# Optimization experiments

Measured on AMD Instinct MI355X. Metric: run time of the kernel, lower is better.

## Reference

```python
import jax, jax.numpy as jnp
import numpy as np

N = 12000       # num nodes
E = 384000      # num edges (avg degree 32)
F_IN = 512      # num_feats
H = 64          # gnn_hid_dim (== anchor_dim)
C = 7           # num_cls
SIGMA = 1.0


def setup_inputs() -> dict:
    key = jax.random.key(0)
    ks = jax.random.split(key, 9)
    scale = lambda fan_in: 1.0 / np.sqrt(fan_in)
    return {
        "x": jax.random.normal(ks[0], (N, F_IN), dtype=jnp.float32),
        "W1": jax.random.normal(ks[1], (F_IN, H), dtype=jnp.float32) * scale(F_IN),
        "b1": jnp.zeros((H,), dtype=jnp.float32),
        "W2": jax.random.normal(ks[2], (H, H), dtype=jnp.float32) * scale(H),
        "b2": jnp.zeros((H,), dtype=jnp.float32),
        "aux": jax.random.normal(ks[3], (H,), dtype=jnp.float32),
        "clf_W": jax.random.normal(ks[4], (2 * H, C), dtype=jnp.float32) * scale(2 * H),
        "clf_b": jnp.zeros((C,), dtype=jnp.float32),
        "edge_index": jax.random.randint(ks[5], (2, E), 0, N, dtype=jnp.int64),
    }


def gcn_conv(x, W, b, src, dst, n):
    # GCNConv: D^{-1/2} (A + I) D^{-1/2} X W + b, with self-loops
    h = x @ W                                                   # [N, out]
    deg = jax.ops.segment_sum(jnp.ones(src.shape[0], h.dtype), dst,
                              num_segments=n) + 1.0             # +1 for self-loop
    inv_sqrt = jax.lax.rsqrt(deg)
    norm = inv_sqrt[src] * inv_sqrt[dst]                        # [E]
    agg = jax.ops.segment_sum(h[src] * norm[:, None], dst, num_segments=n)
    agg = agg + h / deg[:, None]                                # self-loop term (norm = 1/deg)
    return agg + b


def reference(x, W1, b1, W2, b2, aux, clf_W, clf_b, edge_index):
    src, dst = edge_index[0], edge_index[1]
    n = x.shape[0]
    h = jax.nn.relu(gcn_conv(x, W1, b1, src, dst, n))
    h = gcn_conv(h, W2, b2, src, dst, n)                        # [N, H]
    # kernel aggregate: pairwise Gaussian kernel on cosine scores
    a = aux / jnp.maximum(jnp.linalg.norm(aux), 1e-12)          # F.normalize
    hn = jnp.maximum(jnp.linalg.norm(h, axis=-1), 1e-8)         # cosine_similarity eps
    score = (h @ a) / hn                                        # [N]
    diff = score[None, :] - score[:, None]                      # [N, N]
    kappa = jnp.exp(-(diff * diff) / (SIGMA * SIGMA))           # [N, N]
    z = (kappa @ h) / jnp.sum(kappa, axis=1, keepdims=True)     # [N, H]
    return jnp.concatenate([h, z], axis=-1) @ clf_W + clf_b     # [N, C]
```

## Files before the change

### kernel.cpp

```cpp
#include <hip/hip_runtime.h>
#include <hip/hip_bf16.h>

#define N_NODES 12000
#define N_EDGES 384000
#define F_IN 512
#define H 64
#define C_CLS 7
#define KTERMS 16
#define PAD 96
#define CSTR 32
#define MOM_BLKS 192
#define NB 4

__device__ __forceinline__ float wred_f(float x) {
    #pragma unroll
    for (int o = 32; o > 0; o >>= 1) x += __shfl_xor(x, o);
    return x;
}

__global__ __launch_bounds__(256) void init_k(int* __restrict__ cur,
                                              double* __restrict__ M,
                                              double* __restrict__ m0) {
    int i = blockIdx.x * 256 + threadIdx.x;
    if (i < N_NODES) cur[i * CSTR] = 0;
    if (i < KTERMS * 64) M[i] = 0.0;
    if (i < KTERMS) m0[i] = 0.0;
}

__global__ __launch_bounds__(256) void k1_gemm_fill(const float* __restrict__ x,
                                                    const float* __restrict__ W1,
                                                    const int* __restrict__ ei,
                                                    float* __restrict__ hbuf,
                                                    int* __restrict__ cur,
                                                    int* __restrict__ csrc) {
    const int b = blockIdx.x, t = threadIdx.x;
    if (b < 750) {
        __shared__ float xsT[64 * 19];
        __shared__ float wsm[64 * 64];
        const int tx = t & 15, ty = t >> 4;
        const int i0 = b * 16;
        float acc[4] = {};
        for (int k0 = 0; k0 < F_IN; k0 += 64) {
            {
                float4 v = *(const float4*)(x + (size_t)(i0 + ty) * F_IN + k0 + tx * 4);
                xsT[(tx * 4 + 0) * 19 + ty] = v.x;
                xsT[(tx * 4 + 1) * 19 + ty] = v.y;
                xsT[(tx * 4 + 2) * 19 + ty] = v.z;
                xsT[(tx * 4 + 3) * 19 + ty] = v.w;
            }
            #pragma unroll
            for (int q = 0; q < 4; ++q) {
                int idx = t + q * 256;
                int r = idx >> 4, c4 = idx & 15;
                *(float4*)(&wsm[r * 64 + c4 * 4]) =
                    *(const float4*)(W1 + (size_t)(k0 + r) * H + c4 * 4);
            }
            __syncthreads();
            #pragma unroll
            for (int kk = 0; kk < 64; ++kk) {
                float a = xsT[kk * 19 + ty];
                float4 bb = *(const float4*)(&wsm[kk * 64 + tx * 4]);
                acc[0] += a * bb.x; acc[1] += a * bb.y;
                acc[2] += a * bb.z; acc[3] += a * bb.w;
            }
            __syncthreads();
        }
        *(float4*)(hbuf + (size_t)(i0 + ty) * H + tx * 4) =
            make_float4(acc[0], acc[1], acc[2], acc[3]);
    } else {
        for (int e = (b - 750) * 256 + t; e < N_EDGES; e += 250 * 256) {
            int s = ei[e];
            int d = ei[N_EDGES + e];
            int pos = atomicAdd(&cur[d * CSTR], 1);
            if (pos < PAD) csrc[d * PAD + pos] = s;
        }
    }
}

__global__ __launch_bounds__(256) void agg1_k(const float* __restrict__ hbuf,
                                              const float* __restrict__ b1,
                                              const int* __restrict__ cur,
                                              const int* __restrict__ csrc,
                                              float* __restrict__ h1) {
    __shared__ int2 sPair[NB * PAD];
    __shared__ int sDeg[NB];
    __shared__ float sIsd[NB];
    const int t = threadIdx.x, f = t & 63, w = t >> 6;
    const int base = blockIdx.x * NB;
    if (t < NB) {
        int d = cur[(base + t) * CSTR];
        sDeg[t] = min(d, PAD);
        sIsd[t] = rsqrtf((float)d + 1.f);
    }
    __syncthreads();
    for (int idx = t; idx < NB * PAD; idx += 256) {
        int n = idx / PAD, e = idx - n * PAD;
        if (e < sDeg[n]) {
            int s = csrc[(base + n) * PAD + e];
            float ws_ = rsqrtf((float)cur[s * CSTR] + 1.f);
            sPair[idx] = make_int2(s, __float_as_int(ws_));
        }
    }
    __syncthreads();
    const int i = base + w;
    const int deg = sDeg[w];
    const float isd = sIsd[w];
    const int2* pp = sPair + w * PAD;
    float acc = 0.f;
    int e = 0;
    for (; e + 4 <= deg; e += 4) {
        int2 p0 = pp[e], p1 = pp[e + 1], p2 = pp[e + 2], p3 = pp[e + 3];
        acc += hbuf[p0.x * H + f] * __int_as_float(p0.y)
             + hbuf[p1.x * H + f] * __int_as_float(p1.y)
             + hbuf[p2.x * H + f] * __int_as_float(p2.y)
             + hbuf[p3.x * H + f] * __int_as_float(p3.y);
    }
    for (; e < deg; ++e) {
        int2 p = pp[e];
        acc += hbuf[p.x * H + f] * __int_as_float(p.y);
    }
    float res = (acc + hbuf[i * H + f] * isd) * isd + b1[f];
    h1[i * H + f] = fmaxf(res, 0.f);
}

__global__ __launch_bounds__(256) void agg2_k(const float* __restrict__ h1,
                                              const float* __restrict__ W2,
                                              const float* __restrict__ b2,
                                              const float* __restrict__ aux,
                                              const int* __restrict__ cur,
                                              const int* __restrict__ csrc,
                                              float* __restrict__ h2,
                                              float* __restrict__ score) {
    __shared__ float w2s[64 * 64];
    __shared__ int2 sPair[NB * PAD];
    __shared__ int sDeg[NB];
    __shared__ float sIsd[NB];
    __shared__ float anorm[64];
    __shared__ float gsh[NB * 64];
    const int t = threadIdx.x, f = t & 63, w = t >> 6;
    const int base = blockIdx.x * NB;
    #pragma unroll
    for (int q = 0; q < 4; ++q) {
        int idx = t + q * 256;
        int r = idx >> 4, c4 = idx & 15;
        *(float4*)(&w2s[r * 64 + c4 * 4]) = *(const float4*)(W2 + r * H + c4 * 4);
    }
    if (t < NB) {
        int d = cur[(base + t) * CSTR];
        sDeg[t] = min(d, PAD);
        sIsd[t] = rsqrtf((float)d + 1.f);
    }
    if (t < 64) {
        float av = aux[t];
        anorm[t] = av * rsqrtf(fmaxf(wred_f(av * av), 1e-24f));
    }
    __syncthreads();
    for (int idx = t; idx < NB * PAD; idx += 256) {
        int n = idx / PAD, e = idx - n * PAD;
        if (e < sDeg[n]) {
            int s = csrc[(base + n) * PAD + e];
            float ws_ = rsqrtf((float)cur[s * CSTR] + 1.f);
            sPair[idx] = make_int2(s, __float_as_int(ws_));
        }
    }
    __syncthreads();
    const int i = base + w;
    const int deg = sDeg[w];
    const float isd = sIsd[w];
    const int2* pp = sPair + w * PAD;
    float acc = 0.f;
    int e = 0;
    for (; e + 4 <= deg; e += 4) {
        int2 p0 = pp[e], p1 = pp[e + 1], p2 = pp[e + 2], p3 = pp[e + 3];
        acc += h1[p0.x * H + f] * __int_as_float(p0.y)
             + h1[p1.x * H + f] * __int_as_float(p1.y)
             + h1[p2.x * H + f] * __int_as_float(p2.y)
             + h1[p3.x * H + f] * __int_as_float(p3.y);
    }
    for (; e < deg; ++e) {
        int2 p = pp[e];
        acc += h1[p.x * H + f] * __int_as_float(p.y);
    }
    float g = (acc + h1[i * H + f] * isd) * isd;
    gsh[w * 64 + f] = g;
    __builtin_amdgcn_wave_barrier();
    float hv = b2[f];
    #pragma unroll 16
    for (int k = 0; k < 64; ++k) hv += gsh[w * 64 + k] * w2s[k * 64 + f];
    h2[i * H + f] = hv;
    float dp = wred_f(hv * anorm[f]);
    float nn = wred_f(hv * hv);
    if (f == 0) score[i] = dp / fmaxf(sqrtf(nn), 1e-8f);
}

__global__ __launch_bounds__(256) void momden_k(const float* __restrict__ h2,
                                                const float* __restrict__ score,
                                                double* __restrict__ M,
                                                double* __restrict__ m0) {
    const int t = threadIdx.x, f = t & 63, g = t >> 6;
    float accM[KTERMS], accD[KTERMS];
    #pragma unroll
    for (int k = 0; k < KTERMS; ++k) { accM[k] = 0.f; accD[k] = 0.f; }
    for (int j = blockIdx.x * 4 + g; j < N_NODES; j += MOM_BLKS * 4) {
        float sj = score[j];
        float wj = expf(-sj * sj);
        float hv = h2[j * H + f];
        float tm = wj * hv, td = wj;
        #pragma unroll
        for (int k = 0; k < KTERMS; ++k) {
            accM[k] += tm; tm *= sj;
            accD[k] += td; td *= sj;
        }
    }
    __shared__ float Msh[4 * KTERMS * 64];
    __shared__ float Dsh[4 * KTERMS];
    #pragma unroll
    for (int k = 0; k < KTERMS; ++k) Msh[(g * KTERMS + k) * 64 + f] = accM[k];
    if (f == 0) {
        #pragma unroll
        for (int k = 0; k < KTERMS; ++k) Dsh[g * KTERMS + k] = accD[k];
    }
    __syncthreads();
    for (int idx = t; idx < KTERMS * 64; idx += 256) {
        int k = idx >> 6, ff = idx & 63;
        float sum = Msh[(0 * KTERMS + k) * 64 + ff] + Msh[(1 * KTERMS + k) * 64 + ff]
                  + Msh[(2 * KTERMS + k) * 64 + ff] + Msh[(3 * KTERMS + k) * 64 + ff];
        unsafeAtomicAdd(&M[idx], (double)sum);
    }
    if (t < KTERMS) {
        float sum = Dsh[t] + Dsh[KTERMS + t] + Dsh[2 * KTERMS + t] + Dsh[3 * KTERMS + t];
        unsafeAtomicAdd(&m0[t], (double)sum);
    }
}

__global__ __launch_bounds__(256) void final_k(const float* __restrict__ h2,
                                               const float* __restrict__ score,
                                               const double* __restrict__ M,
                                               const double* __restrict__ m0,
                                               const float* __restrict__ clfW,
                                               const float* __restrict__ clfb,
                                               float* __restrict__ out) {
    __shared__ float Ms[KTERMS * 64];
    __shared__ float m0s[KTERMS];
    __shared__ float cw[128 * C_CLS];
    __shared__ float cb[8];
    __shared__ float zh[4 * 128];
    const int t = threadIdx.x, f = t & 63, w = t >> 6;
    for (int idx = t; idx < KTERMS * 64; idx += 256) Ms[idx] = (float)M[idx];
    if (t < KTERMS) m0s[t] = (float)m0[t];
    for (int idx = t; idx < 128 * C_CLS; idx += 256) cw[idx] = clfW[idx];
    if (t < C_CLS) cb[t] = clfb[t];
    __syncthreads();
    const int base = blockIdx.x * 16;
    for (int q = 0; q < 4; ++q) {
        int i = base + q * 4 + w;
        float s = score[i];
        float c = expf(-s * s);
        float t2 = 2.f * s;
        float num = 0.f, den = 0.f;
        #pragma unroll
        for (int k = 0; k < KTERMS; ++k) {
            num += c * Ms[k * 64 + f];
            den += c * m0s[k];
            c *= t2 * (1.0f / (float)(k + 1));
        }
        zh[w * 128 + f] = h2[i * H + f];
        zh[w * 128 + 64 + f] = num / den;
        __builtin_amdgcn_wave_barrier();
        if (f < C_CLS) {
            float o = cb[f];
            #pragma unroll 8
            for (int u = 0; u < 128; ++u) o += zh[w * 128 + u] * cw[u * C_CLS + f];
            out[(size_t)i * C_CLS + f] = o;
        }
        __builtin_amdgcn_wave_barrier();
    }
}

extern "C" void kernel_launch(void* const* d_in, const int* in_sizes, int n_in,
                              void* d_out, int out_size, void* d_ws, size_t ws_size,
                              hipStream_t stream) {
    (void)in_sizes; (void)n_in; (void)out_size; (void)ws_size;
    const float* x    = (const float*)d_in[0];
    const float* W1   = (const float*)d_in[1];
    const float* b1   = (const float*)d_in[2];
    const float* W2   = (const float*)d_in[3];
    const float* b2   = (const float*)d_in[4];
    const float* aux  = (const float*)d_in[5];
    const float* clfW = (const float*)d_in[6];
    const float* clfb = (const float*)d_in[7];
    const int*   ei   = (const int*)d_in[8];
    float* out = (float*)d_out;
    char* ws = (char*)d_ws;

    float*  hbuf  = (float*)(ws + 0);
    float*  h1    = (float*)(ws + 3072000);
    float*  h2    = (float*)(ws + 6144000);
    float*  score = (float*)(ws + 9216000);
    int*    csrc  = (int*)  (ws + 9264000);
    int*    cur   = (int*)  (ws + 13872000);
    double* M     = (double*)(ws + 15408000);
    double* m0    = (double*)(ws + 15416192);

    init_k<<<47, 256, 0, stream>>>(cur, M, m0);
    k1_gemm_fill<<<1000, 256, 0, stream>>>(x, W1, ei, hbuf, cur, csrc);
    agg1_k<<<N_NODES / NB, 256, 0, stream>>>(hbuf, b1, cur, csrc, h1);
    agg2_k<<<N_NODES / NB, 256, 0, stream>>>(h1, W2, b2, aux, cur, csrc, h2, score);
    momden_k<<<MOM_BLKS, 256, 0, stream>>>(h2, score, M, m0);
    final_k<<<750, 256, 0, stream>>>(h2, score, M, m0, clfW, clfb, out);
}
```

Baseline: 95.46 us.

## Register-block the x@W1 GEMM with 4x4 tiles over 64-row blocks

Each GEMM block now covers 64 rows instead of 16, and each thread computes a 4x4 output tile from vectorized shared-memory loads of both x and W1. This raises arithmetic intensity per shared-memory load and loads W1 into shared memory once per 64 rows instead of once per 16, cutting global traffic for W1. The block count falls from 750 to 188, with the edge-fill blocks rebalanced to 256. In exchange there are fewer GEMM blocks to spread across the CUs, more registers per thread, and a clamp/guard for the partial last tile.

```diff
diff --git a/kernel.cpp b/kernel.cpp
--- a/kernel.cpp
+++ b/kernel.cpp
@@ -11,6 +11,9 @@
 #define CSTR 32
 #define MOM_BLKS 192
 #define NB 4
+#define GEMM_BLKS 188
+#define FILL_BLKS 256
+#define XS_STR 68
 
 __device__ __forceinline__ float wred_f(float x) {
     #pragma unroll
@@ -34,41 +37,71 @@
                                                     int* __restrict__ cur,
                                                     int* __restrict__ csrc) {
     const int b = blockIdx.x, t = threadIdx.x;
-    if (b < 750) {
-        __shared__ float xsT[64 * 19];
+    if (b < GEMM_BLKS) {
+        __shared__ float xs[64 * XS_STR];
         __shared__ float wsm[64 * 64];
         const int tx = t & 15, ty = t >> 4;
-        const int i0 = b * 16;
-        float acc[4] = {};
+        const int i0 = b * 64;
+        float acc[4][4] = {};
         for (int k0 = 0; k0 < F_IN; k0 += 64) {
-            {
-                float4 v = *(const float4*)(x + (size_t)(i0 + ty) * F_IN + k0 + tx * 4);
-                xsT[(tx * 4 + 0) * 19 + ty] = v.x;
-                xsT[(tx * 4 + 1) * 19 + ty] = v.y;
-                xsT[(tx * 4 + 2) * 19 + ty] = v.z;
-                xsT[(tx * 4 + 3) * 19 + ty] = v.w;
+            #pragma unroll
+            for (int q = 0; q < 4; ++q) {
+                int idx = t + q * 256;
+                int row = idx >> 4, kg = idx & 15;
+                int rg = min(i0 + row, N_NODES - 1);
+                *(float4*)(&xs[row * XS_STR + kg * 4]) =
+                    *(const float4*)(x + (size_t)rg * F_IN + k0 + kg * 4);
             }
             #pragma unroll
             for (int q = 0; q < 4; ++q) {
                 int idx = t + q * 256;
-                int r = idx >> 4, c4 = idx & 15;
-                *(float4*)(&wsm[r * 64 + c4 * 4]) =
-                    *(const float4*)(W1 + (size_t)(k0 + r) * H + c4 * 4);
+                int r = idx >> 4, cg = idx & 15;
+                *(float4*)(&wsm[r * 64 + cg * 4]) =
+                    *(const float4*)(W1 + (size_t)(k0 + r) * H + cg * 4);
             }
             __syncthreads();
             #pragma unroll
-            for (int kk = 0; kk < 64; ++kk) {
-                float a = xsT[kk * 19 + ty];
-                float4 bb = *(const float4*)(&wsm[kk * 64 + tx * 4]);
-                acc[0] += a * bb.x; acc[1] += a * bb.y;
-                acc[2] += a * bb.z; acc[3] += a * bb.w;
+            for (int kk0 = 0; kk0 < 64; kk0 += 4) {
+                float4 a0 = *(const float4*)(&xs[(ty * 4 + 0) * XS_STR + kk0]);
+                float4 a1 = *(const float4*)(&xs[(ty * 4 + 1) * XS_STR + kk0]);
+                float4 a2 = *(const float4*)(&xs[(ty * 4 + 2) * XS_STR + kk0]);
+                float4 a3 = *(const float4*)(&xs[(ty * 4 + 3) * XS_STR + kk0]);
+                float4 b0 = *(const float4*)(&wsm[(kk0 + 0) * 64 + tx * 4]);
+                float4 b1 = *(const float4*)(&wsm[(kk0 + 1) * 64 + tx * 4]);
+                float4 b2 = *(const float4*)(&wsm[(kk0 + 2) * 64 + tx * 4]);
+                float4 b3 = *(const float4*)(&wsm[(kk0 + 3) * 64 + tx * 4]);
+                #define MAC4(AV, BV) \
+                    acc[0][0] += AV.x * BV.x; acc[0][1] += AV.x * BV.y; \
+                    acc[0][2] += AV.x * BV.z; acc[0][3] += AV.x * BV.w;
+                acc[0][0] += a0.x * b0.x; acc[0][1] += a0.x * b0.y; acc[0][2] += a0.x * b0.z; acc[0][3] += a0.x * b0.w;
+                acc[0][0] += a0.y * b1.x; acc[0][1] += a0.y * b1.y; acc[0][2] += a0.y * b1.z; acc[0][3] += a0.y * b1.w;
+                acc[0][0] += a0.z * b2.x; acc[0][1] += a0.z * b2.y; acc[0][2] += a0.z * b2.z; acc[0][3] += a0.z * b2.w;
+                acc[0][0] += a0.w * b3.x; acc[0][1] += a0.w * b3.y; acc[0][2] += a0.w * b3.z; acc[0][3] += a0.w * b3.w;
+                acc[1][0] += a1.x * b0.x; acc[1][1] += a1.x * b0.y; acc[1][2] += a1.x * b0.z; acc[1][3] += a1.x * b0.w;
+                acc[1][0] += a1.y * b1.x; acc[1][1] += a1.y * b1.y; acc[1][2] += a1.y * b1.z; acc[1][3] += a1.y * b1.w;
+                acc[1][0] += a1.z * b2.x; acc[1][1] += a1.z * b2.y; acc[1][2] += a1.z * b2.z; acc[1][3] += a1.z * b2.w;
+                acc[1][0] += a1.w * b3.x; acc[1][1] += a1.w * b3.y; acc[1][2] += a1.w * b3.z; acc[1][3] += a1.w * b3.w;
+                acc[2][0] += a2.x * b0.x; acc[2][1] += a2.x * b0.y; acc[2][2] += a2.x * b0.z; acc[2][3] += a2.x * b0.w;
+                acc[2][0] += a2.y * b1.x; acc[2][1] += a2.y * b1.y; acc[2][2] += a2.y * b1.z; acc[2][3] += a2.y * b1.w;
+                acc[2][0] += a2.z * b2.x; acc[2][1] += a2.z * b2.y; acc[2][2] += a2.z * b2.z; acc[2][3] += a2.z * b2.w;
+                acc[2][0] += a2.w * b3.x; acc[2][1] += a2.w * b3.y; acc[2][2] += a2.w * b3.z; acc[2][3] += a2.w * b3.w;
+                acc[3][0] += a3.x * b0.x; acc[3][1] += a3.x * b0.y; acc[3][2] += a3.x * b0.z; acc[3][3] += a3.x * b0.w;
+                acc[3][0] += a3.y * b1.x; acc[3][1] += a3.y * b1.y; acc[3][2] += a3.y * b1.z; acc[3][3] += a3.y * b1.w;
+                acc[3][0] += a3.z * b2.x; acc[3][1] += a3.z * b2.y; acc[3][2] += a3.z * b2.z; acc[3][3] += a3.z * b2.w;
+                acc[3][0] += a3.w * b3.x; acc[3][1] += a3.w * b3.y; acc[3][2] += a3.w * b3.z; acc[3][3] += a3.w * b3.w;
+                #undef MAC4
             }
             __syncthreads();
         }
-        *(float4*)(hbuf + (size_t)(i0 + ty) * H + tx * 4) =
-            make_float4(acc[0], acc[1], acc[2], acc[3]);
+        #pragma unroll
+        for (int r = 0; r < 4; ++r) {
+            int row = i0 + ty * 4 + r;
+            if (row < N_NODES)
+                *(float4*)(hbuf + (size_t)row * H + tx * 4) =
+                    make_float4(acc[r][0], acc[r][1], acc[r][2], acc[r][3]);
+        }
     } else {
-        for (int e = (b - 750) * 256 + t; e < N_EDGES; e += 250 * 256) {
+        for (int e = (b - GEMM_BLKS) * 256 + t; e < N_EDGES; e += FILL_BLKS * 256) {
             int s = ei[e];
             int d = ei[N_EDGES + e];
             int pos = atomicAdd(&cur[d * CSTR], 1);
@@ -303,7 +336,7 @@
     double* m0    = (double*)(ws + 15416192);
 
     init_k<<<47, 256, 0, stream>>>(cur, M, m0);
-    k1_gemm_fill<<<1000, 256, 0, stream>>>(x, W1, ei, hbuf, cur, csrc);
+    k1_gemm_fill<<<GEMM_BLKS + FILL_BLKS, 256, 0, stream>>>(x, W1, ei, hbuf, cur, csrc);
     agg1_k<<<N_NODES / NB, 256, 0, stream>>>(hbuf, b1, cur, csrc, h1);
     agg2_k<<<N_NODES / NB, 256, 0, stream>>>(h1, W2, b2, aux, cur, csrc, h2, score);
     momden_k<<<MOM_BLKS, 256, 0, stream>>>(h2, score, M, m0);
```

After: 96.48 us. About the same (+1.1%).
